# Optimization experiments

Measured on AMD Instinct MI355X. Metric: run time of the kernel, lower is better.

Reference implementation:

```python
import jax, jax.numpy as jnp
import numpy as np

NUM_BANDS = 24
HID = 128
B = 8
T = 800
L = 192000


def _hann(K):
    # torch.hann_window default is periodic
    n = np.arange(K)
    return 0.5 * (1.0 - np.cos(2.0 * np.pi * n / K))


def _make_filter_bank(num_bands=NUM_BANDS, K=31):
    half = K // 2
    d = (np.arange(K) - half).astype(np.float64)
    ds = np.where(d == 0, 1.0, d)
    win = _hann(K)
    W = np.zeros((num_bands, 1, K), np.float64)
    for i in range(num_bands):
        cf = 100.0 + i * 7000.0 / num_bands
        w = np.where(d == 0, 1.0, np.sin(2.0 * np.pi * cf * ds / 24000.0) / (np.pi * ds + 1e-8))
        w = w * win
        w = w / (np.abs(w).sum() + 1e-8)
        W[i, 0] = w
    return jnp.asarray(W, jnp.float32)


def _make_noise_type_filters(K=63):
    half = K // 2
    d = (np.arange(K) - half).astype(np.float64)
    ds = np.where(d == 0, 1.0, d)
    win = _hann(K)
    f0 = np.where(d == 0, 1.0, -0.85 * np.sin(np.pi * ds / K) / (np.pi * ds + 1e-8))
    f1 = np.where(d == 0, 1.0, np.sin(np.pi * ds / (K / 2)) / (np.pi * ds + 1e-8) * np.exp(-np.abs(ds) / 5.0))
    f2 = np.sin(np.pi * d / (K * 2)) / np.maximum(1.0, np.pi * d)
    f3 = np.sin(np.pi * d / (K / 4)) / np.maximum(1.0, np.pi * d) * np.exp(-np.abs(d) / 10.0)
    F = np.stack([f0, f1, f2, f3], 0)
    F = F * win[None, :]
    F = F / (np.abs(F).sum(axis=1, keepdims=True) + 1e-8)
    return jnp.asarray(F[:, None, :], jnp.float32)  # [4,1,K]


def conv1d(x, w, pad):
    # x: [B,Cin,L], w: [Cout,Cin,K]; cross-correlation like torch Conv1d
    return jax.lax.conv_general_dilated(x, w, (1,), [(pad, pad)],
                                        dimension_numbers=('NCH', 'OIH', 'NCH'))


def linterp(x, L_out):
    # F.interpolate(mode='linear', align_corners=False) over last axis
    T_in = x.shape[-1]
    pos = (jnp.arange(L_out, dtype=x.dtype) + 0.5) * (T_in / L_out) - 0.5
    pos = jnp.clip(pos, 0.0, T_in - 1)
    i0 = jnp.floor(pos).astype(jnp.int32)
    i1 = jnp.minimum(i0 + 1, T_in - 1)
    w = pos - i0
    return jnp.take(x, i0, axis=-1) * (1.0 - w) + jnp.take(x, i1, axis=-1) * w


def _noise_gate(intensity, attack_rate):
    # intensity, attack_rate: [B,L]; audio_length > 4 always here
    diff = jnp.pad(intensity[:, 1:] - intensity[:, :-1], ((0, 0), (1, 0)))
    attack_mask = (diff > 0.1).astype(intensity.dtype)
    enhanced = jnp.clip(intensity + attack_mask * attack_rate * 0.3, 0.0, 1.0)
    inc = (diff > 0).astype(intensity.dtype)
    gate = intensity * (1.0 - inc) + enhanced * inc
    g = jnp.pad(gate, ((0, 0), (2, 2)), mode='reflect')[:, None, :]
    k = jnp.ones((1, 1, 5), gate.dtype) / 5.0
    return conv1d(g, k, 0)[:, 0, :]


def setup_inputs() -> dict:
    key = jax.random.key(0)
    ks = jax.random.split(key, 8)
    s = 0.05
    inp = {
        'condition': jax.random.normal(ks[0], (B, HID, T), jnp.float32),
        'white_noise': jax.random.normal(ks[1], (B, 1, L), jnp.float32),
        'np_w1': jax.random.normal(ks[2], (256, HID, 3), jnp.float32) * s,
        'np_b1': jnp.zeros((256,), jnp.float32),
        'np_w2': jax.random.normal(ks[3], (256, 256, 3), jnp.float32) * s,
        'np_b2': jnp.zeros((256,), jnp.float32),
        'np_w3': jax.random.normal(ks[4], (NUM_BANDS + 3, 256, 1), jnp.float32) * s,
        'np_b3': jnp.zeros((NUM_BANDS + 3,), jnp.float32),
        'ss_w1': jax.random.normal(ks[5], (128, HID, 3), jnp.float32) * s,
        'ss_b1': jnp.zeros((128,), jnp.float32),
        'ss_w2': jax.random.normal(ks[6], (4, 128, 1), jnp.float32) * s,
        'ss_b2': jnp.zeros((4,), jnp.float32),
        'fb_w': _make_filter_bank(),
        'nt_w': _make_noise_type_filters(),
        'audio_length': L,
    }
    return inp


def reference(condition, white_noise, np_w1, np_b1, np_w2, np_b2, np_w3, np_b3,
              ss_w1, ss_b1, ss_w2, ss_b2, fb_w, nt_w, audio_length):
    # noise predictor
    h = jax.nn.leaky_relu(conv1d(condition, np_w1, 1) + np_b1[None, :, None], 0.1)
    h = jax.nn.leaky_relu(conv1d(h, np_w2, 1) + np_b2[None, :, None], 0.1)
    noise_params = conv1d(h, np_w3, 0) + np_b3[None, :, None]  # [B,27,T]
    band_amps = jax.nn.sigmoid(noise_params[:, :NUM_BANDS])
    attack = jax.nn.sigmoid(noise_params[:, -3]) * 10.0
    release = jax.nn.sigmoid(noise_params[:, -2]) * 5.0  # computed but unused (as in source)
    intensity = jax.nn.sigmoid(noise_params[:, -1])
    # spectral shaper
    g = jax.nn.leaky_relu(conv1d(condition, ss_w1, 1) + ss_b1[None, :, None], 0.1)
    ntw = jax.nn.softmax(conv1d(g, ss_w2, 0) + ss_b2[None, :, None], axis=1)  # [B,4,T]
    # upsample frame-rate controls to sample rate
    band_up = linterp(band_amps, audio_length)   # [B,24,L]
    ntw_up = linterp(ntw, audio_length)          # [B,4,L]
    inten_up = linterp(intensity, audio_length)  # [B,L]
    attack_up = linterp(attack, audio_length)
    _release_up = linterp(release, audio_length)
    # noise-type filter bank (4 filters stacked as one conv)
    ftypes = conv1d(white_noise, nt_w, 31)                       # [B,4,L]
    filtered = jnp.sum(ftypes * ntw_up, axis=1, keepdims=True)   # [B,1,L]
    # 24-band filter bank stacked as one conv
    bands = conv1d(filtered, fb_w, 15)                           # [B,24,L]
    shaped = jnp.sum(bands * band_up, axis=1)                    # [B,L]
    gate = _noise_gate(inten_up, attack_up)
    return shaped * gate, gate
```

## Files before the change

### kernel.cpp

```cpp
#include <hip/hip_runtime.h>
#include <math.h>

static constexpr int B  = 8;
static constexpr int T  = 800;
static constexpr int L  = 192000;
static constexpr int NB = 24;
static constexpr float SCALE = 800.0f / 192000.0f;

typedef __bf16 bf8 __attribute__((ext_vector_type(8)));
typedef float  f4  __attribute__((ext_vector_type(4)));

__device__ __forceinline__ float sigf(float x) { return 1.0f / (1.0f + __expf(-x)); }
__device__ __forceinline__ float leaky(float x) { return x >= 0.0f ? x : 0.1f * x; }
__device__ __forceinline__ unsigned short f2bf(float f) {
    unsigned u = __float_as_uint(f);
    u = u + 0x7FFFu + ((u >> 16) & 1u);
    return (unsigned short)(u >> 16);
}
__device__ __forceinline__ float bflo(unsigned u) { return __uint_as_float(u << 16); }
__device__ __forceinline__ float bfhi(unsigned u) { return __uint_as_float(u & 0xffff0000u); }

__device__ __forceinline__ void interp_idx(int l, int& i0, int& i1, float& w) {
    float pos = ((float)l + 0.5f) * SCALE - 0.5f;
    pos = fminf(fmaxf(pos, 0.0f), (float)(T - 1));
    i0 = (int)pos;
    i1 = min(i0 + 1, T - 1);
    w = pos - (float)i0;
}

__global__ __launch_bounds__(256) void k_twm(const float* __restrict__ w1,
                                             const float* __restrict__ w2,
                                             const float* __restrict__ wss,
                                             unsigned short* __restrict__ wT1,
                                             unsigned short* __restrict__ wT2,
                                             unsigned short* __restrict__ wTs) {
    int idx = blockIdx.x * 256 + threadIdx.x;
    if (idx < 98304) {
        int tap = idx / (256 * 128), r = idx % (256 * 128);
        int cout = r / 128, cin = r % 128;
        wT1[idx] = f2bf(w1[(cout * 128 + cin) * 3 + tap]);
    } else if (idx < 98304 + 196608) {
        int j = idx - 98304;
        int tap = j / (256 * 256), r = j % (256 * 256);
        int cout = r / 256, cin = r % 256;
        wT2[j] = f2bf(w2[(cout * 256 + cin) * 3 + tap]);
    } else if (idx < 98304 + 196608 + 49152) {
        int j = idx - 294912;
        int tap = j / (128 * 128), r = j % (128 * 128);
        int cout = r / 128, cin = r % 128;
        wTs[j] = f2bf(wss[(cout * 128 + cin) * 3 + tap]);
    }
}

union SMem {
    struct {
        unsigned short xs[50 * 136];
        unsigned short h1s[34 * 264];
        unsigned short h2s[32 * 264];
        float bnd[32][25];
    } np;
    struct {
        unsigned short xs[34 * 136];
        unsigned short gs[32 * 136];
        float sv[32][5];
        float nws[32][5];
    } ss;
};

__global__ __launch_bounds__(512) void k_mega(const float* __restrict__ cond,
                                              const unsigned short* __restrict__ wT1,
                                              const float* __restrict__ b1,
                                              const unsigned short* __restrict__ wT2,
                                              const float* __restrict__ b2np,
                                              const float* __restrict__ w3,
                                              const float* __restrict__ b3,
                                              const float* __restrict__ fbw,
                                              const unsigned short* __restrict__ wTs,
                                              const float* __restrict__ bss,
                                              const float* __restrict__ w2ss,
                                              const float* __restrict__ b2ss,
                                              const float* __restrict__ ntf,
                                              float* __restrict__ h_all,
                                              float* __restrict__ g_all,
                                              float* __restrict__ attack,
                                              float* __restrict__ inten) {
    __shared__ SMem sm;
    const int b = blockIdx.y;
    const int t0 = blockIdx.x * 32;
    const int tid = threadIdx.x;
    const int wave = tid >> 6, lane = tid & 63;
    const int nfr = lane & 15;
    const int ko8 = (lane >> 4) * 8;
    const int rb = (lane >> 4) * 4;
    const int tcol = lane & 15;

    if (blockIdx.z == 0) {
        for (int i = tid; i < 50 * 128; i += 512) {
            int cin = i / 50, j = i % 50;
            int t = t0 - 2 + j;
            sm.np.xs[j * 136 + cin] = (t >= 0 && t < T) ? f2bf(cond[(b * 128 + cin) * T + t])
                                                        : (unsigned short)0;
        }
        __syncthreads();
        const int coutb = wave * 32;
        f4 a1[3][2] = {};
#pragma unroll
        for (int tap = 0; tap < 3; ++tap) {
            bf8 aw[2][4];
#pragma unroll
            for (int m = 0; m < 2; ++m)
#pragma unroll
                for (int q = 0; q < 4; ++q)
                    aw[m][q] = *reinterpret_cast<const bf8*>(
                        wT1 + ((tap * 256 + coutb + m * 16 + nfr) * 128 + q * 32 + ko8));
#pragma unroll
            for (int q = 0; q < 4; ++q) {
                bf8 bv0 = *reinterpret_cast<const bf8*>(&sm.np.xs[(nfr + tap) * 136 + q * 32 + ko8]);
                bf8 bv1 = *reinterpret_cast<const bf8*>(&sm.np.xs[(nfr + 16 + tap) * 136 + q * 32 + ko8]);
                bf8 bv2 = *reinterpret_cast<const bf8*>(&sm.np.xs[(nfr + 32 + tap) * 136 + q * 32 + ko8]);
#pragma unroll
                for (int m = 0; m < 2; ++m) {
                    a1[0][m] = __builtin_amdgcn_mfma_f32_16x16x32_bf16(aw[m][q], bv0, a1[0][m], 0, 0, 0);
                    a1[1][m] = __builtin_amdgcn_mfma_f32_16x16x32_bf16(aw[m][q], bv1, a1[1][m], 0, 0, 0);
                    a1[2][m] = __builtin_amdgcn_mfma_f32_16x16x32_bf16(aw[m][q], bv2, a1[2][m], 0, 0, 0);
                }
            }
        }
#pragma unroll
        for (int nt = 0; nt < 3; ++nt) {
            int lcol = nt * 16 + tcol;
            if (lcol < 34) {
                int gcol = t0 - 1 + lcol;
                bool ok = (gcol >= 0 && gcol < T);
#pragma unroll
                for (int m = 0; m < 2; ++m) {
                    ushort4 pk;
                    if (ok) {
                        pk.x = f2bf(leaky(a1[nt][m][0] + b1[coutb + m * 16 + rb + 0]));
                        pk.y = f2bf(leaky(a1[nt][m][1] + b1[coutb + m * 16 + rb + 1]));
                        pk.z = f2bf(leaky(a1[nt][m][2] + b1[coutb + m * 16 + rb + 2]));
                        pk.w = f2bf(leaky(a1[nt][m][3] + b1[coutb + m * 16 + rb + 3]));
                    } else {
                        pk.x = pk.y = pk.z = pk.w = 0;
                    }
                    *reinterpret_cast<ushort4*>(&sm.np.h1s[lcol * 264 + coutb + m * 16 + rb]) = pk;
                }
            }
        }
        __syncthreads();
        f4 a2[2][2] = {};
#pragma unroll
        for (int tap = 0; tap < 3; ++tap) {
            bf8 aw[2][8];
#pragma unroll
            for (int m = 0; m < 2; ++m)
#pragma unroll
                for (int q = 0; q < 8; ++q)
                    aw[m][q] = *reinterpret_cast<const bf8*>(
                        wT2 + ((tap * 256 + coutb + m * 16 + nfr) * 256 + q * 32 + ko8));
#pragma unroll
            for (int q = 0; q < 8; ++q) {
                bf8 bv0 = *reinterpret_cast<const bf8*>(&sm.np.h1s[(nfr + tap) * 264 + q * 32 + ko8]);
                bf8 bv1 = *reinterpret_cast<const bf8*>(&sm.np.h1s[(nfr + 16 + tap) * 264 + q * 32 + ko8]);
#pragma unroll
                for (int m = 0; m < 2; ++m) {
                    a2[0][m] = __builtin_amdgcn_mfma_f32_16x16x32_bf16(aw[m][q], bv0, a2[0][m], 0, 0, 0);
                    a2[1][m] = __builtin_amdgcn_mfma_f32_16x16x32_bf16(aw[m][q], bv1, a2[1][m], 0, 0, 0);
                }
            }
        }
#pragma unroll
        for (int nv = 0; nv < 2; ++nv)
#pragma unroll
            for (int m = 0; m < 2; ++m) {
                ushort4 pk;
                pk.x = f2bf(leaky(a2[nv][m][0] + b2np[coutb + m * 16 + rb + 0]));
                pk.y = f2bf(leaky(a2[nv][m][1] + b2np[coutb + m * 16 + rb + 1]));
                pk.z = f2bf(leaky(a2[nv][m][2] + b2np[coutb + m * 16 + rb + 2]));
                pk.w = f2bf(leaky(a2[nv][m][3] + b2np[coutb + m * 16 + rb + 3]));
                *reinterpret_cast<ushort4*>(&sm.np.h2s[(nv * 16 + tcol) * 264 + coutb + m * 16 + rb]) = pk;
            }
        __syncthreads();
        for (int i = tid; i < 27 * 32; i += 512) {
            int c = i >> 5, t = i & 31;
            float s = b3[c];
            const unsigned short* hp = &sm.np.h2s[t * 264];
            const float* wp3 = w3 + c * 256;
#pragma unroll 4
            for (int kk = 0; kk < 256; kk += 8) {
                uint4 u = *reinterpret_cast<const uint4*>(hp + kk);
                float4 wa = *reinterpret_cast<const float4*>(wp3 + kk);
                float4 wb = *reinterpret_cast<const float4*>(wp3 + kk + 4);
                s += bflo(u.x) * wa.x + bfhi(u.x) * wa.y
                   + bflo(u.y) * wa.z + bfhi(u.y) * wa.w
                   + bflo(u.z) * wb.x + bfhi(u.z) * wb.y
                   + bflo(u.w) * wb.z + bfhi(u.w) * wb.w;
            }
            if (c < 24) sm.np.bnd[t][c] = sigf(s);
            else if (c == 24) attack[b * T + t0 + t] = sigf(s) * 10.0f;
            else if (c == 26) inten[b * T + t0 + t] = sigf(s);
        }
        __syncthreads();
        for (int i = tid; i < 31 * 32; i += 512) {
            int k = i >> 5, t = i & 31;
            float s = 0.0f;
#pragma unroll
            for (int c = 0; c < NB; ++c) s += sm.np.bnd[t][c] * fbw[c * 31 + k];
            h_all[(b * 31 + k) * T + t0 + t] = s;
        }
    } else {
        for (int i = tid; i < 34 * 128; i += 512) {
            int cin = i / 34, tr = i % 34;
            int t = t0 + tr - 1;
            sm.ss.xs[tr * 136 + cin] = (t >= 0 && t < T) ? f2bf(cond[(b * 128 + cin) * T + t])
                                                         : (unsigned short)0;
        }
        __syncthreads();
        const int coutb = wave * 16;
        f4 acc[2] = {};
#pragma unroll
        for (int tap = 0; tap < 3; ++tap) {
            bf8 aw[4];
#pragma unroll
            for (int q = 0; q < 4; ++q)
                aw[q] = *reinterpret_cast<const bf8*>(
                    wTs + ((tap * 128 + coutb + nfr) * 128 + q * 32 + ko8));
#pragma unroll
            for (int q = 0; q < 4; ++q) {
                bf8 bv0 = *reinterpret_cast<const bf8*>(&sm.ss.xs[(nfr + tap) * 136 + q * 32 + ko8]);
                bf8 bv1 = *reinterpret_cast<const bf8*>(&sm.ss.xs[(nfr + 16 + tap) * 136 + q * 32 + ko8]);
                acc[0] = __builtin_amdgcn_mfma_f32_16x16x32_bf16(aw[q], bv0, acc[0], 0, 0, 0);
                acc[1] = __builtin_amdgcn_mfma_f32_16x16x32_bf16(aw[q], bv1, acc[1], 0, 0, 0);
            }
        }
#pragma unroll
        for (int nv = 0; nv < 2; ++nv) {
            ushort4 pk;
            pk.x = f2bf(leaky(acc[nv][0] + bss[coutb + rb + 0]));
            pk.y = f2bf(leaky(acc[nv][1] + bss[coutb + rb + 1]));
            pk.z = f2bf(leaky(acc[nv][2] + bss[coutb + rb + 2]));
            pk.w = f2bf(leaky(acc[nv][3] + bss[coutb + rb + 3]));
            *reinterpret_cast<ushort4*>(&sm.ss.gs[(nv * 16 + tcol) * 136 + coutb + rb]) = pk;
        }
        __syncthreads();
        if (tid < 128) {
            int c = tid & 3, tl = tid >> 2;
            float s = b2ss[c];
#pragma unroll
            for (int kk = 0; kk < 128; kk += 8) {
                uint4 u = *reinterpret_cast<const uint4*>(&sm.ss.gs[tl * 136 + kk]);
                float4 wa = *reinterpret_cast<const float4*>(&w2ss[c * 128 + kk]);
                float4 wb = *reinterpret_cast<const float4*>(&w2ss[c * 128 + kk + 4]);
                s += bflo(u.x) * wa.x + bfhi(u.x) * wa.y
                   + bflo(u.y) * wa.z + bfhi(u.y) * wa.w
                   + bflo(u.z) * wb.x + bfhi(u.z) * wb.y
                   + bflo(u.w) * wb.z + bfhi(u.w) * wb.w;
            }
            sm.ss.sv[tl][c] = s;
        }
        __syncthreads();
        if (tid < 32) {
            float a0 = sm.ss.sv[tid][0], a1v = sm.ss.sv[tid][1];
            float a2v = sm.ss.sv[tid][2], a3v = sm.ss.sv[tid][3];
            float m = fmaxf(fmaxf(a0, a1v), fmaxf(a2v, a3v));
            float e0 = __expf(a0 - m), e1 = __expf(a1v - m);
            float e2 = __expf(a2v - m), e3 = __expf(a3v - m);
            float inv = 1.0f / (e0 + e1 + e2 + e3);
            sm.ss.nws[tid][0] = e0 * inv; sm.ss.nws[tid][1] = e1 * inv;
            sm.ss.nws[tid][2] = e2 * inv; sm.ss.nws[tid][3] = e3 * inv;
        }
        __syncthreads();
        for (int i = tid; i < 63 * 32; i += 512) {
            int k = i >> 5, t = i & 31;
            float s = sm.ss.nws[t][0] * ntf[k] + sm.ss.nws[t][1] * ntf[63 + k]
                    + sm.ss.nws[t][2] * ntf[126 + k] + sm.ss.nws[t][3] * ntf[189 + k];
            g_all[(b * 63 + k) * T + t0 + t] = s;
        }
    }
}

__device__ __forceinline__ float interp_T(const float* __restrict__ a, int b, int p) {
    int i0, i1; float w;
    interp_idx(p, i0, i1, w);
    return a[b * T + i0] * (1.0f - w) + a[b * T + i1] * w;
}

__device__ __forceinline__ int refl(int p) {
    return p < 0 ? -p : (p >= L ? 2 * L - 2 - p : p);
}

__global__ __launch_bounds__(256) void k_sr(const float* __restrict__ wn,
                                            const float* __restrict__ g_all,
                                            const float* __restrict__ h_all,
                                            const float* __restrict__ attack,
                                            const float* __restrict__ inten,
                                            float* __restrict__ out) {
    __shared__ float wns[348];
    __shared__ float gl[4][63];
    __shared__ float hl[4][31];
    __shared__ float flt[286];
    __shared__ float ipl[261];
    __shared__ float gp[260];
    const int b = blockIdx.y;
    const int l0 = blockIdx.x * 256;
    const int tid = threadIdx.x;
    for (int i = tid; i < 348; i += 256) {
        int p = l0 - 46 + i;
        wns[i] = (p >= 0 && p < L) ? wn[b * L + p] : 0.0f;
    }
    int fg0, fgu; float wgu;
    interp_idx(l0 - 15, fg0, fgu, wgu);
    for (int i = tid; i < 376; i += 256) {
        if (i < 252) {
            int j = i / 63, k = i % 63;
            int f = min(fg0 + j, T - 1);
            gl[j][k] = g_all[(b * 63 + k) * T + f];
        } else {
            int j2 = (i - 252) / 31, k2 = (i - 252) % 31;
            int f = min(fg0 + j2, T - 1);
            hl[j2][k2] = h_all[(b * 31 + k2) * T + f];
        }
    }
    for (int i = tid; i < 261; i += 256)
        ipl[i] = interp_T(inten, b, l0 - 3 + i);
    __syncthreads();
    for (int i = tid; i < 260; i += 256) {
        int p = l0 - 2 + i;
        int pr = refl(p);
        float cur = ipl[pr - l0 + 3];
        float prev = (pr == 0) ? cur : ipl[pr - 1 - l0 + 3];
        float diff = cur - prev;
        float ar = interp_T(attack, b, pr);
        float enh = fminf(fmaxf(cur + (diff > 0.1f ? ar * 0.3f : 0.0f), 0.0f), 1.0f);
        gp[i] = (diff > 0.0f) ? enh : cur;
    }
    for (int i = tid; i < 286; i += 256) {
        int p = l0 - 15 + i;
        float v = 0.0f;
        if (p >= 0 && p < L) {
            int i0, i1; float w;
            interp_idx(p, i0, i1, w);
            int d0 = min(max(i0 - fg0, 0), 3);
            int d1 = min(max(i1 - fg0, 0), 3);
            float a0 = 0.0f, a1 = 0.0f;
#pragma unroll
            for (int k = 0; k < 63; ++k) {
                float xk = wns[i + k];
                a0 += xk * gl[d0][k];
                a1 += xk * gl[d1][k];
            }
            v = (1.0f - w) * a0 + w * a1;
        }
        flt[i] = v;
    }
    __syncthreads();
    const int l = l0 + tid;
    int i0, i1; float w;
    interp_idx(l, i0, i1, w);
    int d0 = min(max(i0 - fg0, 0), 3);
    int d1 = min(max(i1 - fg0, 0), 3);
    float a0 = 0.0f, a1 = 0.0f;
#pragma unroll
    for (int k = 0; k < 31; ++k) {
        float xk = flt[tid + k];
        a0 += xk * hl[d0][k];
        a1 += xk * hl[d1][k];
    }
    float shaped = (1.0f - w) * a0 + w * a1;
    float g5 = (gp[tid] + gp[tid + 1] + gp[tid + 2] + gp[tid + 3] + gp[tid + 4]) * 0.2f;
    out[b * L + l] = shaped * g5;
    out[B * L + b * L + l] = g5;
}

extern "C" void kernel_launch(void* const* d_in, const int* in_sizes, int n_in,
                              void* d_out, int out_size, void* d_ws, size_t ws_size,
                              hipStream_t stream) {
    const float* cond  = (const float*)d_in[0];
    const float* wn    = (const float*)d_in[1];
    const float* np_w1 = (const float*)d_in[2];
    const float* np_b1 = (const float*)d_in[3];
    const float* np_w2 = (const float*)d_in[4];
    const float* np_b2 = (const float*)d_in[5];
    const float* np_w3 = (const float*)d_in[6];
    const float* np_b3 = (const float*)d_in[7];
    const float* ss_w1 = (const float*)d_in[8];
    const float* ss_b1 = (const float*)d_in[9];
    const float* ss_w2 = (const float*)d_in[10];
    const float* ss_b2 = (const float*)d_in[11];
    const float* fb_w  = (const float*)d_in[12];
    const float* nt_w  = (const float*)d_in[13];

    char* p = (char*)d_ws;
    unsigned short* wT1 = (unsigned short*)p; p += 196608;
    unsigned short* wT2 = (unsigned short*)p; p += 393216;
    unsigned short* wTs = (unsigned short*)p; p += 98304;
    float* attack = (float*)p; p += 25600;
    float* inten  = (float*)p; p += 25600;
    float* g_all  = (float*)p; p += 1612800;
    float* h_all  = (float*)p; p += 793600;
    float* out = (float*)d_out;

    k_twm<<<1344, 256, 0, stream>>>(np_w1, np_w2, ss_w1, wT1, wT2, wTs);
    k_mega<<<dim3(25, 8, 2), 512, 0, stream>>>(cond, wT1, np_b1, wT2, np_b2, np_w3, np_b3,
                                               fb_w, wTs, ss_b1, ss_w2, ss_b2, nt_w,
                                               h_all, g_all, attack, inten);
    k_sr<<<dim3(750, 8), 256, 0, stream>>>(wn, g_all, h_all, attack, inten, out);
}
```

Measured before the change: 159.0 us.

## Double k_sr tile to 512 samples, vectorize filter reads, flatten k_mega grid

The sample-rate kernel now handles 512 outputs per block instead of 256. That halves the halo overhead for the noise window and the filter-row loads, and it needs five frame rows of the interpolated filters instead of four. The inner convolution loops read filter coefficients as float2 pairs from padded shared rows, which cuts LDS instruction count. The mega kernel grid is flattened to 1D with batch in the low bits, changing the block scheduling order. Larger blocks raise LDS and register use per block, which may reduce occupancy.

```diff
diff --git a/kernel.cpp b/kernel.cpp
--- a/kernel.cpp
+++ b/kernel.cpp
@@ -85,8 +85,11 @@
                                               float* __restrict__ attack,
                                               float* __restrict__ inten) {
     __shared__ SMem sm;
-    const int b = blockIdx.y;
-    const int t0 = blockIdx.x * 32;
+    const int bx = blockIdx.x;
+    const int b = bx & 7;
+    const int quad = bx >> 3;
+    const int chain = quad & 1;
+    const int t0 = (quad >> 1) * 32;
     const int tid = threadIdx.x;
     const int wave = tid >> 6, lane = tid & 63;
     const int nfr = lane & 15;
@@ -94,7 +97,7 @@
     const int rb = (lane >> 4) * 4;
     const int tcol = lane & 15;
 
-    if (blockIdx.z == 0) {
+    if (chain == 0) {
         for (int i = tid; i < 50 * 128; i += 512) {
             int cin = i / 50, j = i % 50;
             int t = t0 - 2 + j;
@@ -289,42 +292,43 @@
     return p < 0 ? -p : (p >= L ? 2 * L - 2 - p : p);
 }
 
-__global__ __launch_bounds__(256) void k_sr(const float* __restrict__ wn,
+__global__ __launch_bounds__(512) void k_sr(const float* __restrict__ wn,
                                             const float* __restrict__ g_all,
                                             const float* __restrict__ h_all,
                                             const float* __restrict__ attack,
                                             const float* __restrict__ inten,
                                             float* __restrict__ out) {
-    __shared__ float wns[348];
-    __shared__ float gl[4][63];
-    __shared__ float hl[4][31];
-    __shared__ float flt[286];
-    __shared__ float ipl[261];
-    __shared__ float gp[260];
+    __shared__ float wns[604];
+    __shared__ float gl[5][64];
+    __shared__ float hl[5][32];
+    __shared__ float flt[542];
+    __shared__ float ipl[517];
+    __shared__ float gp[516];
     const int b = blockIdx.y;
-    const int l0 = blockIdx.x * 256;
+    const int l0 = blockIdx.x * 512;
     const int tid = threadIdx.x;
-    for (int i = tid; i < 348; i += 256) {
+    for (int i = tid; i < 604; i += 512) {
         int p = l0 - 46 + i;
         wns[i] = (p >= 0 && p < L) ? wn[b * L + p] : 0.0f;
     }
     int fg0, fgu; float wgu;
     interp_idx(l0 - 15, fg0, fgu, wgu);
-    for (int i = tid; i < 376; i += 256) {
-        if (i < 252) {
+    for (int i = tid; i < 470; i += 512) {
+        if (i < 315) {
             int j = i / 63, k = i % 63;
             int f = min(fg0 + j, T - 1);
             gl[j][k] = g_all[(b * 63 + k) * T + f];
         } else {
-            int j2 = (i - 252) / 31, k2 = (i - 252) % 31;
+            int i2 = i - 315;
+            int j2 = i2 / 31, k2 = i2 % 31;
             int f = min(fg0 + j2, T - 1);
             hl[j2][k2] = h_all[(b * 31 + k2) * T + f];
         }
     }
-    for (int i = tid; i < 261; i += 256)
+    for (int i = tid; i < 517; i += 512)
         ipl[i] = interp_T(inten, b, l0 - 3 + i);
     __syncthreads();
-    for (int i = tid; i < 260; i += 256) {
+    for (int i = tid; i < 516; i += 512) {
         int p = l0 - 2 + i;
         int pr = refl(p);
         float cur = ipl[pr - l0 + 3];
@@ -334,20 +338,30 @@
         float enh = fminf(fmaxf(cur + (diff > 0.1f ? ar * 0.3f : 0.0f), 0.0f), 1.0f);
         gp[i] = (diff > 0.0f) ? enh : cur;
     }
-    for (int i = tid; i < 286; i += 256) {
+    for (int i = tid; i < 542; i += 512) {
         int p = l0 - 15 + i;
         float v = 0.0f;
         if (p >= 0 && p < L) {
             int i0, i1; float w;
             interp_idx(p, i0, i1, w);
-            int d0 = min(max(i0 - fg0, 0), 3);
-            int d1 = min(max(i1 - fg0, 0), 3);
+            int d0 = min(max(i0 - fg0, 0), 4);
+            int d1 = min(max(i1 - fg0, 0), 4);
             float a0 = 0.0f, a1 = 0.0f;
-#pragma unroll
-            for (int k = 0; k < 63; ++k) {
-                float xk = wns[i + k];
-                a0 += xk * gl[d0][k];
-                a1 += xk * gl[d1][k];
+            const float* g0r = gl[d0];
+            const float* g1r = gl[d1];
+#pragma unroll
+            for (int kp = 0; kp < 31; ++kp) {
+                int k = kp * 2;
+                float2 G0 = *reinterpret_cast<const float2*>(g0r + k);
+                float2 G1 = *reinterpret_cast<const float2*>(g1r + k);
+                float x0 = wns[i + k], x1 = wns[i + k + 1];
+                a0 += x0 * G0.x; a0 += x1 * G0.y;
+                a1 += x0 * G1.x; a1 += x1 * G1.y;
+            }
+            {
+                float x = wns[i + 62];
+                a0 += x * g0r[62];
+                a1 += x * g1r[62];
             }
             v = (1.0f - w) * a0 + w * a1;
         }
@@ -357,14 +371,24 @@
     const int l = l0 + tid;
     int i0, i1; float w;
     interp_idx(l, i0, i1, w);
-    int d0 = min(max(i0 - fg0, 0), 3);
-    int d1 = min(max(i1 - fg0, 0), 3);
+    int d0 = min(max(i0 - fg0, 0), 4);
+    int d1 = min(max(i1 - fg0, 0), 4);
     float a0 = 0.0f, a1 = 0.0f;
-#pragma unroll
-    for (int k = 0; k < 31; ++k) {
-        float xk = flt[tid + k];
-        a0 += xk * hl[d0][k];
-        a1 += xk * hl[d1][k];
+    const float* h0r = hl[d0];
+    const float* h1r = hl[d1];
+#pragma unroll
+    for (int kp = 0; kp < 15; ++kp) {
+        int k = kp * 2;
+        float2 H0 = *reinterpret_cast<const float2*>(h0r + k);
+        float2 H1 = *reinterpret_cast<const float2*>(h1r + k);
+        float x0 = flt[tid + k], x1 = flt[tid + k + 1];
+        a0 += x0 * H0.x; a0 += x1 * H0.y;
+        a1 += x0 * H1.x; a1 += x1 * H1.y;
+    }
+    {
+        float x = flt[tid + 30];
+        a0 += x * h0r[30];
+        a1 += x * h1r[30];
     }
     float shaped = (1.0f - w) * a0 + w * a1;
     float g5 = (gp[tid] + gp[tid + 1] + gp[tid + 2] + gp[tid + 3] + gp[tid + 4]) * 0.2f;
@@ -401,8 +425,8 @@
     float* out = (float*)d_out;
 
     k_twm<<<1344, 256, 0, stream>>>(np_w1, np_w2, ss_w1, wT1, wT2, wTs);
-    k_mega<<<dim3(25, 8, 2), 512, 0, stream>>>(cond, wT1, np_b1, wT2, np_b2, np_w3, np_b3,
-                                               fb_w, wTs, ss_b1, ss_w2, ss_b2, nt_w,
-                                               h_all, g_all, attack, inten);
-    k_sr<<<dim3(750, 8), 256, 0, stream>>>(wn, g_all, h_all, attack, inten, out);
-}
+    k_mega<<<400, 512, 0, stream>>>(cond, wT1, np_b1, wT2, np_b2, np_w3, np_b3,
+                                    fb_w, wTs, ss_b1, ss_w2, ss_b2, nt_w,
+                                    h_all, g_all, attack, inten);
+    k_sr<<<dim3(375, 8), 512, 0, stream>>>(wn, g_all, h_all, attack, inten, out);
+}
```

Result: slower. 171.3 us (+7.7%).
